# Optimization experiments

Hardware: AMD Instinct MI355X
Metric: run time of the kernel (lower is better)

Reference implementation:

```python
import jax, jax.numpy as jnp
import numpy as np

B, L = 512, 61440
E_MAX = 128          # max events per window (padded)
THRESHOLD = 0.5      # prob -> binary threshold
IOU_THR = 0.2        # IoU match threshold
LEN_THR = 128        # int(freq*time) = int(256*0.5)


def setup_inputs() -> dict:
    key = jax.random.key(0)
    k1, k2 = jax.random.split(key)
    # block-structured signals -> realistic long, sparse events
    out_blocks = jax.random.uniform(k1, (B, L // 256), dtype=jnp.float32)
    output = jnp.repeat(out_blocks, 256, axis=1)            # [B, L] probs
    tgt_blocks = (jax.random.uniform(k2, (B, L // 512)) > 0.75).astype(jnp.float32)
    target = jnp.repeat(tgt_blocks, 512, axis=1)            # [B, L] binary
    return {"output": output, "target": target}


def _filter_short(b):
    # zero out runs of ones shorter than LEN_THR (ProcessingPostEvent)
    starts = jnp.concatenate([b[:1], ((b[1:] - b[:-1]) == 1).astype(b.dtype)])
    run_id = jnp.cumsum(starts)                              # [L]
    run_len = jax.ops.segment_sum(b, run_id, num_segments=L + 1)
    return b * (run_len[run_id] >= LEN_THR).astype(b.dtype)


def _events(b):
    # binary_to_array: [start, end) pairs, padded to E_MAX with [L, L]
    padded = jnp.concatenate([jnp.zeros(1, b.dtype), b, jnp.zeros(1, b.dtype)])
    d = padded[1:] - padded[:-1]                             # [L+1]
    pos = jnp.arange(L + 1)
    starts = jnp.sort(jnp.where(d == 1, pos, L + 1))[:E_MAX]
    ends = jnp.sort(jnp.where(d == -1, pos, L + 1))[:E_MAX]
    starts = jnp.minimum(starts, L)
    ends = jnp.minimum(ends, L)
    n = (d == 1).sum()
    return starts, ends, n


def _best_match(iou):
    # iou: [E_MAX, E_MAX], invalid entries = -1
    max_col = iou.max(0); idx_col = iou.argmax(0)            # best output row per target col
    max_row = iou.max(1); idx_row = iou.argmax(1)            # best target col per output row
    ar = jnp.arange(E_MAX)
    mutual_row = (idx_col[idx_row] == ar) & (max_row >= IOU_THR)   # [E] rows in mutual match
    mutual_col = (idx_row[idx_col] == ar) & (max_col >= IOU_THR)   # [E] cols in mutual match
    row_one = (~mutual_row) & (max_row >= IOU_THR)
    col_one = (~mutual_col) & (max_col >= IOU_THR)
    onehot_row = (ar[None, :] == idx_row[:, None])           # bm[i, idx_row[i]]
    onehot_col = (ar[:, None] == idx_col[None, :])           # bm[idx_col[j], j]
    ones_m = (onehot_row & row_one[:, None]) | (onehot_col & col_one[None, :])
    kill = mutual_row[:, None] | mutual_col[None, :]         # rows/cols of mutual matches zeroed
    ones_m = ones_m & (~kill)
    tp = mutual_row.sum()                                    # count of '2' marks
    return tp, ones_m


def _per_batch(out_prob, tgt):
    b_out = _filter_short((out_prob >= THRESHOLD).astype(jnp.int32))
    b_tgt = (tgt != 0).astype(jnp.int32)
    s_o, e_o, n_out = _events(b_out)
    s_t, e_t, n_tgt = _events(b_tgt)
    inter = jnp.clip(jnp.minimum(e_o[:, None], e_t[None, :])
                     - jnp.maximum(s_o[:, None], s_t[None, :]), 0)
    la = (e_o - s_o)[:, None]
    lb = (e_t - s_t)[None, :]
    den = jnp.maximum(la + lb - inter, 1)
    valid = (jnp.arange(E_MAX) < n_out)[:, None] & (jnp.arange(E_MAX) < n_tgt)[None, :]
    iou = jnp.where(valid, inter.astype(jnp.float32) / den.astype(jnp.float32), -1.0)
    tp1, ones_m = _best_match(iou)
    # second pass on positions marked '1' (iou elsewhere zeroed in original)
    tp2, _ = _best_match(jnp.where(ones_m, iou, -1.0))
    tp = tp1 + tp2
    t_empty = n_tgt == 0
    o_empty = (~t_empty) & (n_out == 0)
    tp_b = jnp.where(t_empty | o_empty, 0, tp)
    # note: faithful to original (adds output count to FN when target empty, etc.)
    fn_b = jnp.where(t_empty, n_out, jnp.where(o_empty, 0, n_tgt - tp))
    fp_b = jnp.where(t_empty, 0, jnp.where(o_empty, n_tgt, n_out - tp))
    return tp_b, fn_b, fp_b


def reference(output, target):
    tp, fn, fp = jax.vmap(_per_batch)(output, target)
    TP = tp.sum().astype(jnp.float32)
    FN = fn.sum().astype(jnp.float32)
    FP = fp.sum().astype(jnp.float32)
    recall = jnp.where(TP + FN == 0, 0.0, TP / jnp.maximum(TP + FN, 1.0))
    precision = jnp.where(TP + FP == 0, 0.0, TP / jnp.maximum(TP + FP, 1.0))
    f1 = jnp.where(precision + recall == 0, 0.0,
                   2.0 * precision * recall / jnp.maximum(precision + recall, 1e-30))
    return recall, precision, f1
```

## Files before the change

kernel.cpp:

```cpp
#include <hip/hip_runtime.h>

typedef unsigned long long ull;

#define L_LEN 61440
#define NBATCH 512
#define EMAX 128
#define RUNBUF 128
#define NWORDS 960
#define NPADW 1080
#define PADW(w) ((w) + ((w) >> 3))
#define NTHREADS 768
#define IOU_THRESH 0.2f
#define LEN_THRESH 128
#define PADPK 0xF000F000u

__device__ __forceinline__ unsigned int mask16_ge(float4 a, float4 b, float4 c, float4 d, float thr) {
    unsigned int m = 0;
    m |= (a.x >= thr) ? 0x0001u : 0u; m |= (a.y >= thr) ? 0x0002u : 0u;
    m |= (a.z >= thr) ? 0x0004u : 0u; m |= (a.w >= thr) ? 0x0008u : 0u;
    m |= (b.x >= thr) ? 0x0010u : 0u; m |= (b.y >= thr) ? 0x0020u : 0u;
    m |= (b.z >= thr) ? 0x0040u : 0u; m |= (b.w >= thr) ? 0x0080u : 0u;
    m |= (c.x >= thr) ? 0x0100u : 0u; m |= (c.y >= thr) ? 0x0200u : 0u;
    m |= (c.z >= thr) ? 0x0400u : 0u; m |= (c.w >= thr) ? 0x0800u : 0u;
    m |= (d.x >= thr) ? 0x1000u : 0u; m |= (d.y >= thr) ? 0x2000u : 0u;
    m |= (d.z >= thr) ? 0x4000u : 0u; m |= (d.w >= thr) ? 0x8000u : 0u;
    return m;
}

__device__ __forceinline__ unsigned int mask16_ne0(float4 a, float4 b, float4 c, float4 d) {
    unsigned int m = 0;
    m |= (a.x != 0.0f) ? 0x0001u : 0u; m |= (a.y != 0.0f) ? 0x0002u : 0u;
    m |= (a.z != 0.0f) ? 0x0004u : 0u; m |= (a.w != 0.0f) ? 0x0008u : 0u;
    m |= (b.x != 0.0f) ? 0x0010u : 0u; m |= (b.y != 0.0f) ? 0x0020u : 0u;
    m |= (b.z != 0.0f) ? 0x0040u : 0u; m |= (b.w != 0.0f) ? 0x0080u : 0u;
    m |= (c.x != 0.0f) ? 0x0100u : 0u; m |= (c.y != 0.0f) ? 0x0200u : 0u;
    m |= (c.z != 0.0f) ? 0x0400u : 0u; m |= (c.w != 0.0f) ? 0x0800u : 0u;
    m |= (d.x != 0.0f) ? 0x1000u : 0u; m |= (d.y != 0.0f) ? 0x2000u : 0u;
    m |= (d.z != 0.0f) ? 0x4000u : 0u; m |= (d.w != 0.0f) ? 0x8000u : 0u;
    return m;
}

__device__ __forceinline__ float iou_pk(unsigned int pk, int ms, int me, int ml) {
    int s = (int)(pk & 0xffffu), e = (int)(pk >> 16);
    int lo = me < e ? me : e;
    int hi = ms > s ? ms : s;
    int inter = lo - hi; if (inter < 0) inter = 0;
    int den = ml + (e - s) - inter; if (den < 1) den = 1;
    return (float)inter / (float)den;
}

#define LOAD8(A0,A1,A2,A3,B0,B1,B2,B3, IT) { \
    const float4* po_ = (const float4*)(op + (IT) * 12288 + tid * 16); \
    const float4* pt_ = (const float4*)(tg + (IT) * 12288 + tid * 16); \
    A0 = po_[0]; A1 = po_[1]; A2 = po_[2]; A3 = po_[3]; \
    B0 = pt_[0]; B1 = pt_[1]; B2 = pt_[2]; B3 = pt_[3]; }

#define PROC(IT, A0,A1,A2,A3,B0,B1,B2,B3) { \
    unsigned int mo_ = mask16_ge(A0, A1, A2, A3, 0.5f); \
    unsigned int mt_ = mask16_ne0(B0, B1, B2, B3); \
    unsigned int u_ = (IT) * NTHREADS + tid; \
    unsigned int pu_ = u_ + ((u_ >> 5) << 2); \
    bmo16[pu_] = (unsigned short)mo_; \
    bmt16[pu_] = (unsigned short)mt_; }

__global__ __launch_bounds__(NTHREADS, 6) void event_f1_kernel(
        const float* __restrict__ outp, const float* __restrict__ tgtp,
        int* __restrict__ per_row) {
    __shared__ ull bm[2][NPADW];
    __shared__ int runs_s[2][RUNBUF], runs_e[2][RUNBUF];
    __shared__ int wtot_s[16], wtot_e[16];
    __shared__ __align__(16) unsigned int pse_o[EMAX], pse_t[EMAX];
    __shared__ int idxr[EMAX], idxc[EMAX];
    __shared__ __align__(16) unsigned int rowfl[EMAX], colfl[EMAX];
    __shared__ int n_out_s, n_tgt_s, ftot0, tp_sh;

    const int tid = threadIdx.x;
    const int lane = tid & 63;
    const int wid = tid >> 6;
    const int row = blockIdx.x;

    const float* op = outp + (size_t)row * L_LEN;
    const float* tg = tgtp + (size_t)row * L_LEN;

    if (tid == 0) tp_sh = 0;

    unsigned short* bmo16 = (unsigned short*)bm[0];
    unsigned short* bmt16 = (unsigned short*)bm[1];
    {
        float4 a0, a1, a2, a3, b0, b1, b2, b3;
        float4 c0, c1, c2, c3, d0, d1, d2, d3;
        LOAD8(a0, a1, a2, a3, b0, b1, b2, b3, 0);
        LOAD8(c0, c1, c2, c3, d0, d1, d2, d3, 1);
        PROC(0, a0, a1, a2, a3, b0, b1, b2, b3);
        LOAD8(a0, a1, a2, a3, b0, b1, b2, b3, 2);
        PROC(1, c0, c1, c2, c3, d0, d1, d2, d3);
        LOAD8(c0, c1, c2, c3, d0, d1, d2, d3, 3);
        PROC(2, a0, a1, a2, a3, b0, b1, b2, b3);
        LOAD8(a0, a1, a2, a3, b0, b1, b2, b3, 4);
        PROC(3, c0, c1, c2, c3, d0, d1, d2, d3);
        PROC(4, a0, a1, a2, a3, b0, b1, b2, b3);
    }
    __syncthreads();

    const int group = tid >> 8;
    const int g = group & 1;
    const int gtid = tid & 255;
    const ull* bmp = bm[g];
    const int w0 = gtid * 4;
    const bool act = (tid < 512) && (gtid < 240);

    ull swm0 = 0, swm1 = 0, swm2 = 0, swm3 = 0;
    ull ewm0 = 0, ewm1 = 0, ewm2 = 0, ewm3 = 0;
    int cs = 0, ce = 0;
    if (act) {
        ull wm1 = (w0 > 0) ? bmp[PADW(w0 - 1)] : 0ull;
        int p0 = PADW(w0);
        ull a = bmp[p0], b = bmp[p0 + 1], c = bmp[p0 + 2], d = bmp[p0 + 3];
        ull wp4 = (w0 + 4 < NWORDS) ? bmp[PADW(w0 + 4)] : 0ull;
        swm0 = a & ~((a << 1) | (wm1 >> 63)); ewm0 = a & ~((a >> 1) | (b << 63));
        swm1 = b & ~((b << 1) | (a >> 63));   ewm1 = b & ~((b >> 1) | (c << 63));
        swm2 = c & ~((c << 1) | (b >> 63));   ewm2 = c & ~((c >> 1) | (d << 63));
        swm3 = d & ~((d << 1) | (c >> 63));   ewm3 = d & ~((d >> 1) | (wp4 << 63));
        cs = __popcll(swm0) + __popcll(swm1) + __popcll(swm2) + __popcll(swm3);
        ce = __popcll(ewm0) + __popcll(ewm1) + __popcll(ewm2) + __popcll(ewm3);
    }
    int incl_s = cs, incl_e = ce;
    #pragma unroll
    for (int d = 1; d < 64; d <<= 1) {
        int us = __shfl_up(incl_s, d, 64);
        int ue = __shfl_up(incl_e, d, 64);
        if (lane >= d) { incl_s += us; incl_e += ue; }
    }
    if (lane == 63) { wtot_s[wid] = incl_s; wtot_e[wid] = incl_e; }
    __syncthreads();
    int off_s = incl_s - cs, off_e = incl_e - ce;
    if (act) {
        for (int wv = (g << 2); wv < wid; ++wv) { off_s += wtot_s[wv]; off_e += wtot_e[wv]; }
        ull m; int base;
        m = swm0; base = w0 * 64;
        while (m) { int z = __builtin_ctzll(m); if (off_s < RUNBUF) runs_s[g][off_s] = base + z; ++off_s; m &= m - 1; }
        m = swm1; base += 64;
        while (m) { int z = __builtin_ctzll(m); if (off_s < RUNBUF) runs_s[g][off_s] = base + z; ++off_s; m &= m - 1; }
        m = swm2; base += 64;
        while (m) { int z = __builtin_ctzll(m); if (off_s < RUNBUF) runs_s[g][off_s] = base + z; ++off_s; m &= m - 1; }
        m = swm3; base += 64;
        while (m) { int z = __builtin_ctzll(m); if (off_s < RUNBUF) runs_s[g][off_s] = base + z; ++off_s; m &= m - 1; }
        m = ewm0; base = w0 * 64;
        while (m) { int z = __builtin_ctzll(m); if (off_e < RUNBUF) runs_e[g][off_e] = base + z + 1; ++off_e; m &= m - 1; }
        m = ewm1; base += 64;
        while (m) { int z = __builtin_ctzll(m); if (off_e < RUNBUF) runs_e[g][off_e] = base + z + 1; ++off_e; m &= m - 1; }
        m = ewm2; base += 64;
        while (m) { int z = __builtin_ctzll(m); if (off_e < RUNBUF) runs_e[g][off_e] = base + z + 1; ++off_e; m &= m - 1; }
        m = ewm3; base += 64;
        while (m) { int z = __builtin_ctzll(m); if (off_e < RUNBUF) runs_e[g][off_e] = base + z + 1; ++off_e; m &= m - 1; }
    }
    __syncthreads();

    const int nro = wtot_s[0] + wtot_s[1] + wtot_s[2] + wtot_s[3];
    const int nrt = wtot_s[4] + wtot_s[5] + wtot_s[6] + wtot_s[7];

    int keep = 0, fs = 0, fe = 0, fincl = 0;
    if (tid < 128) {
        int lim = nro < RUNBUF ? nro : RUNBUF;
        if (tid < lim) { fs = runs_s[0][tid]; fe = runs_e[0][tid]; keep = (fe - fs) >= LEN_THRESH ? 1 : 0; }
        fincl = keep;
        #pragma unroll
        for (int d = 1; d < 64; d <<= 1) {
            int u = __shfl_up(fincl, d, 64);
            if (lane >= d) fincl += u;
        }
        if (tid == 63) ftot0 = fincl;
    } else if (tid < 256) {
        int k = tid - 128;
        int mc = nrt < EMAX ? nrt : EMAX;
        pse_t[k] = (k < mc) ? ((unsigned)runs_s[1][k] | ((unsigned)runs_e[1][k] << 16)) : PADPK;
        if (k == 0) n_tgt_s = nrt;
    }
    __syncthreads();
    if (tid < 128) {
        int off = fincl - keep + (tid >= 64 ? ftot0 : 0);
        if (keep && off < EMAX) pse_o[off] = (unsigned)fs | ((unsigned)fe << 16);
        if (tid == 127) n_out_s = ftot0 + fincl;
    }
    __syncthreads();
    {
        int mcl = n_out_s < EMAX ? n_out_s : EMAX;
        if (tid < 128 && tid >= mcl) pse_o[tid] = PADPK;
    }
    __syncthreads();

    int ntc = n_tgt_s < EMAX ? n_tgt_s : EMAX;
    int noc = n_out_s < EMAX ? n_out_s : EMAX;
    const int nt4 = (ntc + 3) & ~3;
    const int no4 = (noc + 3) & ~3;

    unsigned mypk = PADPK;
    if (tid < 128) mypk = pse_o[tid];
    else if (tid < 256) mypk = pse_t[tid - 128];
    const int my_s = (int)(mypk & 0xffffu);
    const int my_e = (int)(mypk >> 16);
    const int my_len = my_e - my_s;

    float best = -2.0f; int bi = 0;
    if (tid < 128) {
        for (int j = 0; j < nt4; j += 4) {
            uint4 pk = *(const uint4*)&pse_t[j];
            float v0 = iou_pk(pk.x, my_s, my_e, my_len);
            float v1 = iou_pk(pk.y, my_s, my_e, my_len);
            float v2 = iou_pk(pk.z, my_s, my_e, my_len);
            float v3 = iou_pk(pk.w, my_s, my_e, my_len);
            if (v0 > best) { best = v0; bi = j; }
            if (v1 > best) { best = v1; bi = j + 1; }
            if (v2 > best) { best = v2; bi = j + 2; }
            if (v3 > best) { best = v3; bi = j + 3; }
        }
        idxr[tid] = bi;
    } else if (tid < 256) {
        for (int i = 0; i < no4; i += 4) {
            uint4 pk = *(const uint4*)&pse_o[i];
            float v0 = iou_pk(pk.x, my_s, my_e, my_len);
            float v1 = iou_pk(pk.y, my_s, my_e, my_len);
            float v2 = iou_pk(pk.z, my_s, my_e, my_len);
            float v3 = iou_pk(pk.w, my_s, my_e, my_len);
            if (v0 > best) { best = v0; bi = i; }
            if (v1 > best) { best = v1; bi = i + 1; }
            if (v2 > best) { best = v2; bi = i + 2; }
            if (v3 > best) { best = v3; bi = i + 3; }
        }
        idxc[tid - 128] = bi;
    }
    __syncthreads();

    bool mm = false;
    if (tid < 128) mm = (idxc[bi] == tid) && (best >= IOU_THRESH);
    else if (tid < 256) mm = (idxr[bi] == tid - 128) && (best >= IOU_THRESH);
    if (tid < 128) {
        ull bb = __ballot(mm);
        if (lane == 0) atomicAdd(&tp_sh, (int)__popcll(bb));
    }
    __syncthreads();

    const int bi0 = bi;
    const bool m0 = mm;
    const bool one0 = (!mm) && (best >= IOU_THRESH);
    if (tid < 128)      rowfl[tid] = (unsigned)bi0 | (one0 ? 0x100u : 0u) | (m0 ? 0x200u : 0u);
    else if (tid < 256) colfl[tid - 128] = (unsigned)bi0 | (one0 ? 0x100u : 0u) | (m0 ? 0x200u : 0u);
    __syncthreads();

    best = -2.0f; bi = 0;
    if (tid < 128) {
        const int i = tid;
        for (int j = 0; j < nt4; j += 4) {
            uint4 pk = *(const uint4*)&pse_t[j];
            uint4 fl = *(const uint4*)&colfl[j];
            bool om0 = (((j + 0 == bi0) && one0) || ((i == (int)(fl.x & 0xffu)) && (fl.x & 0x100u))) && !m0 && !(fl.x & 0x200u);
            bool om1 = (((j + 1 == bi0) && one0) || ((i == (int)(fl.y & 0xffu)) && (fl.y & 0x100u))) && !m0 && !(fl.y & 0x200u);
            bool om2 = (((j + 2 == bi0) && one0) || ((i == (int)(fl.z & 0xffu)) && (fl.z & 0x100u))) && !m0 && !(fl.z & 0x200u);
            bool om3 = (((j + 3 == bi0) && one0) || ((i == (int)(fl.w & 0xffu)) && (fl.w & 0x100u))) && !m0 && !(fl.w & 0x200u);
            float v0 = om0 ? iou_pk(pk.x, my_s, my_e, my_len) : -1.0f;
            float v1 = om1 ? iou_pk(pk.y, my_s, my_e, my_len) : -1.0f;
            float v2 = om2 ? iou_pk(pk.z, my_s, my_e, my_len) : -1.0f;
            float v3 = om3 ? iou_pk(pk.w, my_s, my_e, my_len) : -1.0f;
            if (v0 > best) { best = v0; bi = j; }
            if (v1 > best) { best = v1; bi = j + 1; }
            if (v2 > best) { best = v2; bi = j + 2; }
            if (v3 > best) { best = v3; bi = j + 3; }
        }
        idxr[tid] = bi;
    } else if (tid < 256) {
        const int j = tid - 128;
        for (int i = 0; i < no4; i += 4) {
            uint4 pk = *(const uint4*)&pse_o[i];
            uint4 fl = *(const uint4*)&rowfl[i];
            bool om0 = (((j == (int)(fl.x & 0xffu)) && (fl.x & 0x100u)) || ((i + 0 == bi0) && one0)) && !(fl.x & 0x200u) && !m0;
            bool om1 = (((j == (int)(fl.y & 0xffu)) && (fl.y & 0x100u)) || ((i + 1 == bi0) && one0)) && !(fl.y & 0x200u) && !m0;
            bool om2 = (((j == (int)(fl.z & 0xffu)) && (fl.z & 0x100u)) || ((i + 2 == bi0) && one0)) && !(fl.z & 0x200u) && !m0;
            bool om3 = (((j == (int)(fl.w & 0xffu)) && (fl.w & 0x100u)) || ((i + 3 == bi0) && one0)) && !(fl.w & 0x200u) && !m0;
            float v0 = om0 ? iou_pk(pk.x, my_s, my_e, my_len) : -1.0f;
            float v1 = om1 ? iou_pk(pk.y, my_s, my_e, my_len) : -1.0f;
            float v2 = om2 ? iou_pk(pk.z, my_s, my_e, my_len) : -1.0f;
            float v3 = om3 ? iou_pk(pk.w, my_s, my_e, my_len) : -1.0f;
            if (v0 > best) { best = v0; bi = i; }
            if (v1 > best) { best = v1; bi = i + 1; }
            if (v2 > best) { best = v2; bi = i + 2; }
            if (v3 > best) { best = v3; bi = i + 3; }
        }
        idxc[tid - 128] = bi;
    }
    __syncthreads();

    mm = false;
    if (tid < 128) mm = (idxc[bi] == tid) && (best >= IOU_THRESH);
    else if (tid < 256) mm = (idxr[bi] == tid - 128) && (best >= IOU_THRESH);
    if (tid < 128) {
        ull bb = __ballot(mm);
        if (lane == 0) atomicAdd(&tp_sh, (int)__popcll(bb));
    }
    __syncthreads();

    if (tid == 0) {
        int n_out = n_out_s, n_tgt = n_tgt_s, tp = tp_sh;
        int tpb, fnb, fpb;
        if (n_tgt == 0)      { tpb = 0;  fnb = n_out;      fpb = 0; }
        else if (n_out == 0) { tpb = 0;  fnb = 0;          fpb = n_tgt; }
        else                 { tpb = tp; fnb = n_tgt - tp; fpb = n_out - tp; }
        per_row[row * 3 + 0] = tpb;
        per_row[row * 3 + 1] = fnb;
        per_row[row * 3 + 2] = fpb;
    }
}

__global__ __launch_bounds__(512) void finalize_kernel(const int* __restrict__ per_row,
                                                       float* __restrict__ out) {
    __shared__ int sm[3][8];
    const int tid = threadIdx.x;
    const int lane = tid & 63;
    const int wid = tid >> 6;
    int tp = per_row[tid * 3 + 0];
    int fn = per_row[tid * 3 + 1];
    int fp = per_row[tid * 3 + 2];
    #pragma unroll
    for (int d = 32; d > 0; d >>= 1) {
        tp += __shfl_down(tp, d, 64);
        fn += __shfl_down(fn, d, 64);
        fp += __shfl_down(fp, d, 64);
    }
    if (lane == 0) { sm[0][wid] = tp; sm[1][wid] = fn; sm[2][wid] = fp; }
    __syncthreads();
    if (tid == 0) {
        int TPi = 0, FNi = 0, FPi = 0;
        #pragma unroll
        for (int w = 0; w < 8; ++w) { TPi += sm[0][w]; FNi += sm[1][w]; FPi += sm[2][w]; }
        float TP = (float)TPi, FN = (float)FNi, FP = (float)FPi;
        float rd = TP + FN;
        float recall = (rd == 0.0f) ? 0.0f : TP / fmaxf(rd, 1.0f);
        float pd = TP + FP;
        float precision = (pd == 0.0f) ? 0.0f : TP / fmaxf(pd, 1.0f);
        float s = precision + recall;
        float f1 = (s == 0.0f) ? 0.0f : 2.0f * precision * recall / fmaxf(s, 1e-30f);
        out[0] = recall; out[1] = precision; out[2] = f1;
    }
}

extern "C" void kernel_launch(void* const* d_in, const int* in_sizes, int n_in,
                              void* d_out, int out_size, void* d_ws, size_t ws_size,
                              hipStream_t stream) {
    const float* outp = (const float*)d_in[0];
    const float* tgtp = (const float*)d_in[1];
    float* res = (float*)d_out;
    int* per_row = (int*)d_ws;

    event_f1_kernel<<<NBATCH, NTHREADS, 0, stream>>>(outp, tgtp, per_row);
    finalize_kernel<<<1, 512, 0, stream>>>(per_row, res);
}
```

Measured before the change: 55.99 us.

## Shrink block to 512 threads with inline-asm pipelined loads and explicit waitcnt

Reduces the block size from 768 to 512 threads, so the load phase becomes seven double-buffered iterations plus a half-block tail. Loads are issued through inline-asm global_load_dwordx4 with explicit s_waitcnt vmcnt and scheduling barriers, to keep the next tile's loads in flight while the current one is processed. The aim is better latency hiding and fewer idle threads in the later phases, which used only 512 threads. The cost is lower occupancy (launch bounds 4) and fragile hand-written waitcnt accounting.

```diff
diff --git a/kernel.cpp b/kernel.cpp
--- a/kernel.cpp
+++ b/kernel.cpp
@@ -1,6 +1,7 @@
 #include <hip/hip_runtime.h>
 
 typedef unsigned long long ull;
+typedef __attribute__((ext_vector_type(4))) float f32x4;
 
 #define L_LEN 61440
 #define NBATCH 512
@@ -9,34 +10,32 @@
 #define NWORDS 960
 #define NPADW 1080
 #define PADW(w) ((w) + ((w) >> 3))
-#define NTHREADS 768
+#define NTHREADS 512
 #define IOU_THRESH 0.2f
 #define LEN_THRESH 128
 #define PADPK 0xF000F000u
 
-__device__ __forceinline__ unsigned int mask16_ge(float4 a, float4 b, float4 c, float4 d, float thr) {
+__device__ __forceinline__ unsigned int mask16v(f32x4 a, f32x4 b, f32x4 c, f32x4 d, bool ge) {
     unsigned int m = 0;
-    m |= (a.x >= thr) ? 0x0001u : 0u; m |= (a.y >= thr) ? 0x0002u : 0u;
-    m |= (a.z >= thr) ? 0x0004u : 0u; m |= (a.w >= thr) ? 0x0008u : 0u;
-    m |= (b.x >= thr) ? 0x0010u : 0u; m |= (b.y >= thr) ? 0x0020u : 0u;
-    m |= (b.z >= thr) ? 0x0040u : 0u; m |= (b.w >= thr) ? 0x0080u : 0u;
-    m |= (c.x >= thr) ? 0x0100u : 0u; m |= (c.y >= thr) ? 0x0200u : 0u;
-    m |= (c.z >= thr) ? 0x0400u : 0u; m |= (c.w >= thr) ? 0x0800u : 0u;
-    m |= (d.x >= thr) ? 0x1000u : 0u; m |= (d.y >= thr) ? 0x2000u : 0u;
-    m |= (d.z >= thr) ? 0x4000u : 0u; m |= (d.w >= thr) ? 0x8000u : 0u;
-    return m;
-}
-
-__device__ __forceinline__ unsigned int mask16_ne0(float4 a, float4 b, float4 c, float4 d) {
-    unsigned int m = 0;
-    m |= (a.x != 0.0f) ? 0x0001u : 0u; m |= (a.y != 0.0f) ? 0x0002u : 0u;
-    m |= (a.z != 0.0f) ? 0x0004u : 0u; m |= (a.w != 0.0f) ? 0x0008u : 0u;
-    m |= (b.x != 0.0f) ? 0x0010u : 0u; m |= (b.y != 0.0f) ? 0x0020u : 0u;
-    m |= (b.z != 0.0f) ? 0x0040u : 0u; m |= (b.w != 0.0f) ? 0x0080u : 0u;
-    m |= (c.x != 0.0f) ? 0x0100u : 0u; m |= (c.y != 0.0f) ? 0x0200u : 0u;
-    m |= (c.z != 0.0f) ? 0x0400u : 0u; m |= (c.w != 0.0f) ? 0x0800u : 0u;
-    m |= (d.x != 0.0f) ? 0x1000u : 0u; m |= (d.y != 0.0f) ? 0x2000u : 0u;
-    m |= (d.z != 0.0f) ? 0x4000u : 0u; m |= (d.w != 0.0f) ? 0x8000u : 0u;
+    if (ge) {
+        m |= (a[0] >= 0.5f) ? 0x0001u : 0u; m |= (a[1] >= 0.5f) ? 0x0002u : 0u;
+        m |= (a[2] >= 0.5f) ? 0x0004u : 0u; m |= (a[3] >= 0.5f) ? 0x0008u : 0u;
+        m |= (b[0] >= 0.5f) ? 0x0010u : 0u; m |= (b[1] >= 0.5f) ? 0x0020u : 0u;
+        m |= (b[2] >= 0.5f) ? 0x0040u : 0u; m |= (b[3] >= 0.5f) ? 0x0080u : 0u;
+        m |= (c[0] >= 0.5f) ? 0x0100u : 0u; m |= (c[1] >= 0.5f) ? 0x0200u : 0u;
+        m |= (c[2] >= 0.5f) ? 0x0400u : 0u; m |= (c[3] >= 0.5f) ? 0x0800u : 0u;
+        m |= (d[0] >= 0.5f) ? 0x1000u : 0u; m |= (d[1] >= 0.5f) ? 0x2000u : 0u;
+        m |= (d[2] >= 0.5f) ? 0x4000u : 0u; m |= (d[3] >= 0.5f) ? 0x8000u : 0u;
+    } else {
+        m |= (a[0] != 0.0f) ? 0x0001u : 0u; m |= (a[1] != 0.0f) ? 0x0002u : 0u;
+        m |= (a[2] != 0.0f) ? 0x0004u : 0u; m |= (a[3] != 0.0f) ? 0x0008u : 0u;
+        m |= (b[0] != 0.0f) ? 0x0010u : 0u; m |= (b[1] != 0.0f) ? 0x0020u : 0u;
+        m |= (b[2] != 0.0f) ? 0x0040u : 0u; m |= (b[3] != 0.0f) ? 0x0080u : 0u;
+        m |= (c[0] != 0.0f) ? 0x0100u : 0u; m |= (c[1] != 0.0f) ? 0x0200u : 0u;
+        m |= (c[2] != 0.0f) ? 0x0400u : 0u; m |= (c[3] != 0.0f) ? 0x0800u : 0u;
+        m |= (d[0] != 0.0f) ? 0x1000u : 0u; m |= (d[1] != 0.0f) ? 0x2000u : 0u;
+        m |= (d[2] != 0.0f) ? 0x4000u : 0u; m |= (d[3] != 0.0f) ? 0x8000u : 0u;
+    }
     return m;
 }
 
@@ -49,26 +48,34 @@
     return (float)inter / (float)den;
 }
 
+#define GLOAD0(dst, p)  asm volatile("global_load_dwordx4 %0, %1, off"            : "=v"(dst) : "v"(p) : "memory")
+#define GLOAD16(dst, p) asm volatile("global_load_dwordx4 %0, %1, off offset:16"  : "=v"(dst) : "v"(p) : "memory")
+#define GLOAD32(dst, p) asm volatile("global_load_dwordx4 %0, %1, off offset:32"  : "=v"(dst) : "v"(p) : "memory")
+#define GLOAD48(dst, p) asm volatile("global_load_dwordx4 %0, %1, off offset:48"  : "=v"(dst) : "v"(p) : "memory")
+
 #define LOAD8(A0,A1,A2,A3,B0,B1,B2,B3, IT) { \
-    const float4* po_ = (const float4*)(op + (IT) * 12288 + tid * 16); \
-    const float4* pt_ = (const float4*)(tg + (IT) * 12288 + tid * 16); \
-    A0 = po_[0]; A1 = po_[1]; A2 = po_[2]; A3 = po_[3]; \
-    B0 = pt_[0]; B1 = pt_[1]; B2 = pt_[2]; B3 = pt_[3]; }
+    const float* po_ = op + (IT) * 8192 + tid * 16; \
+    const float* pt_ = tg + (IT) * 8192 + tid * 16; \
+    GLOAD0(A0, po_); GLOAD16(A1, po_); GLOAD32(A2, po_); GLOAD48(A3, po_); \
+    GLOAD0(B0, pt_); GLOAD16(B1, pt_); GLOAD32(B2, pt_); GLOAD48(B3, pt_); }
+
+#define WAITV(N) { asm volatile("s_waitcnt vmcnt(" #N ")" ::: "memory"); \
+                   __builtin_amdgcn_sched_barrier(0); }
 
 #define PROC(IT, A0,A1,A2,A3,B0,B1,B2,B3) { \
-    unsigned int mo_ = mask16_ge(A0, A1, A2, A3, 0.5f); \
-    unsigned int mt_ = mask16_ne0(B0, B1, B2, B3); \
+    unsigned int mo_ = mask16v(A0, A1, A2, A3, true); \
+    unsigned int mt_ = mask16v(B0, B1, B2, B3, false); \
     unsigned int u_ = (IT) * NTHREADS + tid; \
     unsigned int pu_ = u_ + ((u_ >> 5) << 2); \
     bmo16[pu_] = (unsigned short)mo_; \
     bmt16[pu_] = (unsigned short)mt_; }
 
-__global__ __launch_bounds__(NTHREADS, 6) void event_f1_kernel(
+__global__ __launch_bounds__(NTHREADS, 4) void event_f1_kernel(
         const float* __restrict__ outp, const float* __restrict__ tgtp,
         int* __restrict__ per_row) {
     __shared__ ull bm[2][NPADW];
     __shared__ int runs_s[2][RUNBUF], runs_e[2][RUNBUF];
-    __shared__ int wtot_s[16], wtot_e[16];
+    __shared__ int wtot_s[8], wtot_e[8];
     __shared__ __align__(16) unsigned int pse_o[EMAX], pse_t[EMAX];
     __shared__ int idxr[EMAX], idxc[EMAX];
     __shared__ __align__(16) unsigned int rowfl[EMAX], colfl[EMAX];
@@ -87,27 +94,46 @@
     unsigned short* bmo16 = (unsigned short*)bm[0];
     unsigned short* bmt16 = (unsigned short*)bm[1];
     {
-        float4 a0, a1, a2, a3, b0, b1, b2, b3;
-        float4 c0, c1, c2, c3, d0, d1, d2, d3;
+        f32x4 a0, a1, a2, a3, b0, b1, b2, b3;
+        f32x4 c0, c1, c2, c3, d0, d1, d2, d3;
         LOAD8(a0, a1, a2, a3, b0, b1, b2, b3, 0);
         LOAD8(c0, c1, c2, c3, d0, d1, d2, d3, 1);
-        PROC(0, a0, a1, a2, a3, b0, b1, b2, b3);
+        WAITV(8);  PROC(0, a0, a1, a2, a3, b0, b1, b2, b3);
         LOAD8(a0, a1, a2, a3, b0, b1, b2, b3, 2);
-        PROC(1, c0, c1, c2, c3, d0, d1, d2, d3);
+        WAITV(8);  PROC(1, c0, c1, c2, c3, d0, d1, d2, d3);
         LOAD8(c0, c1, c2, c3, d0, d1, d2, d3, 3);
-        PROC(2, a0, a1, a2, a3, b0, b1, b2, b3);
+        WAITV(8);  PROC(2, a0, a1, a2, a3, b0, b1, b2, b3);
         LOAD8(a0, a1, a2, a3, b0, b1, b2, b3, 4);
-        PROC(3, c0, c1, c2, c3, d0, d1, d2, d3);
-        PROC(4, a0, a1, a2, a3, b0, b1, b2, b3);
-    }
-    __syncthreads();
-
-    const int group = tid >> 8;
-    const int g = group & 1;
+        WAITV(8);  PROC(3, c0, c1, c2, c3, d0, d1, d2, d3);
+        LOAD8(c0, c1, c2, c3, d0, d1, d2, d3, 5);
+        WAITV(8);  PROC(4, a0, a1, a2, a3, b0, b1, b2, b3);
+        LOAD8(a0, a1, a2, a3, b0, b1, b2, b3, 6);
+        WAITV(8);  PROC(5, c0, c1, c2, c3, d0, d1, d2, d3);
+        WAITV(0);  PROC(6, a0, a1, a2, a3, b0, b1, b2, b3);
+    }
+    if (tid < 256) {
+        const float4* po = (const float4*)(op + 57344 + tid * 16);
+        const float4* pt = (const float4*)(tg + 57344 + tid * 16);
+        float4 x0 = po[0], x1 = po[1], x2 = po[2], x3 = po[3];
+        float4 y0 = pt[0], y1 = pt[1], y2 = pt[2], y3 = pt[3];
+        f32x4 fa0 = {x0.x, x0.y, x0.z, x0.w}, fa1 = {x1.x, x1.y, x1.z, x1.w};
+        f32x4 fa2 = {x2.x, x2.y, x2.z, x2.w}, fa3 = {x3.x, x3.y, x3.z, x3.w};
+        f32x4 fb0 = {y0.x, y0.y, y0.z, y0.w}, fb1 = {y1.x, y1.y, y1.z, y1.w};
+        f32x4 fb2 = {y2.x, y2.y, y2.z, y2.w}, fb3 = {y3.x, y3.y, y3.z, y3.w};
+        unsigned int mo = mask16v(fa0, fa1, fa2, fa3, true);
+        unsigned int mt = mask16v(fb0, fb1, fb2, fb3, false);
+        unsigned int u = 3584 + tid;
+        unsigned int pu = u + ((u >> 5) << 2);
+        bmo16[pu] = (unsigned short)mo;
+        bmt16[pu] = (unsigned short)mt;
+    }
+    __syncthreads();
+
+    const int g = tid >> 8;
     const int gtid = tid & 255;
     const ull* bmp = bm[g];
     const int w0 = gtid * 4;
-    const bool act = (tid < 512) && (gtid < 240);
+    const bool act = (gtid < 240);
 
     ull swm0 = 0, swm1 = 0, swm2 = 0, swm3 = 0;
     ull ewm0 = 0, ewm1 = 0, ewm2 = 0, ewm3 = 0;
```

After: 56.48 us. No clear change (+0.9%).
